# Performance work log

Hardware: AMD Instinct MI355X
Metric: run time of the kernel (lower is better)

Reference implementation:

```python
import jax, jax.numpy as jnp
import numpy as np
from jax import lax

B, T, F_IN = 128, 2048, 8
CF = 128   # cnn_filters
H = 96     # lstm_hidden
NC = 6

def _ln(x, g, b, eps=1e-5):
    m = jnp.mean(x, -1, keepdims=True)
    v = jnp.mean((x - m) ** 2, -1, keepdims=True)
    return (x - m) * lax.rsqrt(v + eps) * g + b

def _bn(x, g, b, m, v, eps=1e-5):
    # eval-mode BatchNorm; x is [B,C,T] (channel axis 1) or [B,C]
    if x.ndim == 3:
        return (x - m[None, :, None]) * lax.rsqrt(v + eps)[None, :, None] * g[None, :, None] + b[None, :, None]
    return (x - m) * lax.rsqrt(v + eps) * g + b

def _lstm_scan(xp, whh, bhh, g_hh, b_hh, g_ho, b_ho):
    # xp: [T, B, 4H] = ln_ih(x @ W_ih.T + b_ih), precomputed (LN is per-timestep)
    bsz = xp.shape[1]
    hh = whh.shape[1]
    def step(carry, xt):
        hx, cx = carry
        gates = xt + _ln(hx @ whh.T + bhh, g_hh, b_hh)
        i, f, g, o = jnp.split(gates, 4, axis=-1)  # torch chunk order: in, forget, cell, out
        cy = jax.nn.sigmoid(f) * cx + jax.nn.sigmoid(i) * jnp.tanh(g)
        hy = jax.nn.sigmoid(o) * jnp.tanh(_ln(cy, g_ho, b_ho))
        return (hy, cy), hy
    init = (jnp.zeros((bsz, hh), xp.dtype), jnp.zeros((bsz, hh), xp.dtype))
    _, hs = lax.scan(step, init, xp)
    return hs  # [T, B, H]

def setup_inputs():
    key = jax.random.key(0)
    ks = iter(jax.random.split(key, 64))
    def rn(shape, scale=1.0):
        return jax.random.normal(next(ks), shape, jnp.float32) * scale
    def ru(shape, lo, hi):
        return jax.random.uniform(next(ks), shape, jnp.float32, lo, hi)
    D = 2 * CF  # lstm input size = 256
    d = {}
    d['x'] = rn((B, T, F_IN))
    d['conv1_w'] = rn((CF, F_IN, 7), 1.0 / np.sqrt(F_IN * 7)); d['conv1_b'] = jnp.zeros((CF,))
    d['bn1_g'] = jnp.ones((CF,)); d['bn1_b'] = jnp.zeros((CF,))
    d['bn1_m'] = rn((CF,), 0.1); d['bn1_v'] = ru((CF,), 0.5, 1.5)
    d['conv2_w'] = rn((2 * CF, CF, 5), 1.0 / np.sqrt(CF * 5)); d['conv2_b'] = jnp.zeros((2 * CF,))
    d['bn2_g'] = jnp.ones((2 * CF,)); d['bn2_b'] = jnp.zeros((2 * CF,))
    d['bn2_m'] = rn((2 * CF,), 0.1); d['bn2_v'] = ru((2 * CF,), 0.5, 1.5)
    s = 1.0 / np.sqrt(H)
    for p in ['f', 'b']:
        d[p + 'wih'] = rn((4 * H, D), s); d[p + 'bih'] = rn((4 * H,), s)
        d[p + 'whh'] = rn((4 * H, H), s); d[p + 'bhh'] = rn((4 * H,), s)
        d[p + 'lnih_g'] = jnp.ones((4 * H,)); d[p + 'lnih_b'] = jnp.zeros((4 * H,))
        d[p + 'lnhh_g'] = jnp.ones((4 * H,)); d[p + 'lnhh_b'] = jnp.zeros((4 * H,))
        d[p + 'lnho_g'] = jnp.ones((H,)); d[p + 'lnho_b'] = jnp.zeros((H,))
    d['attn_w'] = rn((1, 2 * H), 1.0 / np.sqrt(2 * H))
    d['fc1_w'] = rn((256, 2 * H), 1.0 / np.sqrt(2 * H)); d['fc1_b'] = jnp.zeros((256,))
    d['bn3_g'] = jnp.ones((256,)); d['bn3_b'] = jnp.zeros((256,))
    d['bn3_m'] = rn((256,), 0.1); d['bn3_v'] = ru((256,), 0.5, 1.5)
    d['fc2_w'] = rn((NC, 256), 1.0 / np.sqrt(256)); d['fc2_b'] = jnp.zeros((NC,))
    return d

def _forward(x, conv1_w, conv1_b, bn1_g, bn1_b, bn1_m, bn1_v,
             conv2_w, conv2_b, bn2_g, bn2_b, bn2_m, bn2_v,
             fwih, fbih, fwhh, fbhh, flnih_g, flnih_b, flnhh_g, flnhh_b, flnho_g, flnho_b,
             bwih, bbih, bwhh, bbhh, blnih_g, blnih_b, blnhh_g, blnhh_b, blnho_g, blnho_b,
             attn_w, fc1_w, fc1_b, bn3_g, bn3_b, bn3_m, bn3_v, fc2_w, fc2_b):
    dn = ('NCH', 'OIH', 'NCH')
    h = jnp.transpose(x, (0, 2, 1))  # [B, F_IN, T]
    h = lax.conv_general_dilated(h, conv1_w, (1,), [(3, 3)], dimension_numbers=dn) + conv1_b[None, :, None]
    h = jax.nn.relu(_bn(h, bn1_g, bn1_b, bn1_m, bn1_v))
    h = lax.reduce_window(h, -jnp.inf, lax.max, (1, 1, 2), (1, 1, 2), 'VALID')
    h = lax.conv_general_dilated(h, conv2_w, (1,), [(2, 2)], dimension_numbers=dn) + conv2_b[None, :, None]
    h = jax.nn.relu(_bn(h, bn2_g, bn2_b, bn2_m, bn2_v))
    h = lax.reduce_window(h, -jnp.inf, lax.max, (1, 1, 2), (1, 1, 2), 'VALID')
    # Dropout(0.3) -> identity at eval
    seq = jnp.transpose(h, (2, 0, 1))  # [T/4, B, 2*CF]
    xp_f = _ln(seq @ fwih.T + fbih, flnih_g, flnih_b)
    hf = _lstm_scan(xp_f, fwhh, fbhh, flnhh_g, flnhh_b, flnho_g, flnho_b)
    xp_b = _ln(seq @ bwih.T + bbih, blnih_g, blnih_b)[::-1]
    hb = _lstm_scan(xp_b, bwhh, bbhh, blnhh_g, blnhh_b, blnho_g, blnho_b)[::-1]
    lstm_out = jnp.transpose(jnp.concatenate([hf, hb], -1), (1, 0, 2))  # [B, T/4, 2H]
    attn = jax.nn.softmax(lstm_out @ attn_w.T, axis=1)  # [B, T/4, 1]
    ctx = jnp.sum(attn * lstm_out, axis=1)  # [B, 2H]
    h2 = jax.nn.relu(_bn(ctx @ fc1_w.T + fc1_b, bn3_g, bn3_b, bn3_m, bn3_v))
    return h2 @ fc2_w.T + fc2_b  # [B, NC]

def reference(x, conv1_w, conv1_b, bn1_g, bn1_b, bn1_m, bn1_v,
              conv2_w, conv2_b, bn2_g, bn2_b, bn2_m, bn2_v,
              fwih, fbih, fwhh, fbhh, flnih_g, flnih_b, flnhh_g, flnhh_b, flnho_g, flnho_b,
              bwih, bbih, bwhh, bbhh, blnih_g, blnih_b, blnhh_g, blnhh_b, blnho_g, blnho_b,
              attn_w, fc1_w, fc1_b, bn3_g, bn3_b, bn3_m, bn3_v, fc2_w, fc2_b):
    return _forward(x, conv1_w, conv1_b, bn1_g, bn1_b, bn1_m, bn1_v,
                    conv2_w, conv2_b, bn2_g, bn2_b, bn2_m, bn2_v,
                    fwih, fbih, fwhh, fbhh, flnih_g, flnih_b, flnhh_g, flnhh_b, flnho_g, flnho_b,
                    bwih, bbih, bwhh, bbhh, blnih_g, blnih_b, blnhh_g, blnhh_b, blnho_g, blnho_b,
                    attn_w, fc1_w, fc1_b, bn3_g, bn3_b, bn3_m, bn3_v, fc2_w, fc2_b)
```

## Files before the change

### kernel.cpp

```cpp
#include <hip/hip_runtime.h>

typedef unsigned short u16;
typedef unsigned int   u32;
typedef __attribute__((ext_vector_type(8))) short bf16x8;
typedef __attribute__((ext_vector_type(4))) float f32x4;

#define DI __device__ __forceinline__

DI float b2f(u16 u){ union{u32 i; float f;} x; x.i = ((u32)u)<<16; return x.f; }
DI u16 f2bf(float f){ union{float f; u32 i;} x; x.f=f; u32 r = x.i + 0x7FFFu + ((x.i>>16)&1u); return (u16)(r>>16); }
DI float sigf(float x){ return 1.0f/(1.0f + __expf(-x)); }
DI float tanh_(float x){ return 1.0f - 2.0f/(__expf(2.0f*x)+1.0f); }
DI float dot4(float4 a, float4 b){ return a.x*b.x + a.y*b.y + a.z*b.z + a.w*b.w; }

__global__ __launch_bounds__(256) void k_conv1(
    const float* __restrict__ x, const float* __restrict__ w,
    const float* __restrict__ cb, const float* __restrict__ bg, const float* __restrict__ bb,
    const float* __restrict__ bm, const float* __restrict__ bv, u16* __restrict__ out)
{
  __shared__ __align__(16) float xs[262*12];
  __shared__ __align__(16) float wl[128*7*8];
  __shared__ float As[128], Ss[128];
  const int tid = threadIdx.x;
  const int tc  = blockIdx.x;
  const int b   = blockIdx.y;
  const int tau0 = tc*256;
  for(int f = tid; f < 262*8; f += 256){
    int tt = f >> 3;
    int ci = f & 7;
    int xg = tau0 - 3 + tt;
    float val = 0.f;
    if(xg >= 0 && xg < 2048) val = x[(b*2048 + xg)*8 + ci];
    xs[tt*12 + ci] = val;
  }
  for(int d = tid; d < 128*7*8; d += 256){
    int co = d / 56; int r = d - co*56; int k = r >> 3; int ci = r & 7;
    wl[d] = w[(co*8 + ci)*7 + k];
  }
  if(tid < 128){
    float a = bg[tid] * rsqrtf(bv[tid] + 1e-5f);
    As[tid] = a;
    Ss[tid] = (cb[tid] - bm[tid])*a + bb[tid];
  }
  __syncthreads();
  const float4* xs4 = (const float4*)xs;
  const float4* wl4 = (const float4*)wl;
  const int p2  = tid & 63;
  const int grp = tid >> 6;
  float4 ra[10], rb[10];
  #pragma unroll
  for(int e=0; e<10; e++){ ra[e] = xs4[(4*p2+e)*3]; rb[e] = xs4[(4*p2+e)*3 + 1]; }
  u32* out32 = (u32*)out;
  for(int i = 0; i < 32; i++){
    const int co = grp*32 + i;
    float a0=0.f, a1=0.f, a2=0.f, a3=0.f;
    #pragma unroll
    for(int k=0;k<7;k++){
      float4 wa = wl4[(co*7+k)*2], wb2 = wl4[(co*7+k)*2+1];
      a0 += dot4(ra[k],   wa) + dot4(rb[k],   wb2);
      a1 += dot4(ra[k+1], wa) + dot4(rb[k+1], wb2);
      a2 += dot4(ra[k+2], wa) + dot4(rb[k+2], wb2);
      a3 += dot4(ra[k+3], wa) + dot4(rb[k+3], wb2);
    }
    const float Ac = As[co], Sc = Ss[co];
    const float y0 = fmaxf(fmaxf(a0*Ac+Sc, a1*Ac+Sc), 0.f);
    const float y1 = fmaxf(fmaxf(a2*Ac+Sc, a3*Ac+Sc), 0.f);
    out32[((b*128 + co)<<9) + tc*64 + p2] = (u32)f2bf(y0) | ((u32)f2bf(y1) << 16);
  }
}

__global__ __launch_bounds__(256) void k_prep(
    const float* __restrict__ w, u16* __restrict__ wp3)
{
  const int f = blockIdx.x*256 + threadIdx.x;
  const int co = f / 640; const int r = f - co*640;
  const int ci = r / 5;   const int k = r - ci*5;
  const float wv = w[f];
  const u16 h0 = f2bf(wv);
  const float r1 = wv - b2f(h0);
  const u16 h1 = f2bf(r1);
  const float r2 = r1 - b2f(h1);
  const u16 h2 = f2bf(r2);
  const int cib = ci >> 5, cl = ci & 31;
  const int base = (k*4 + cib)*10240 + co*40 + cl;
  wp3[base]                = h0;
  wp3[base +   5*4*10240]  = h1;
  wp3[base + 2*5*4*10240]  = h2;
}

__global__ __launch_bounds__(512) void k_conv2(
    const u16* __restrict__ cin, const u16* __restrict__ wp3,
    const float* __restrict__ cb, const float* __restrict__ bg, const float* __restrict__ bb,
    const float* __restrict__ bm, const float* __restrict__ bv, u16* __restrict__ seq)
{
  __shared__ __align__(16) u16 xsT[260*136];
  __shared__ __align__(16) u16 wb[3][256*40];
  __shared__ float As[256], Ss[256];
  const int tid = threadIdx.x;
  const int tc  = blockIdx.x;
  const int b   = blockIdx.y;
  const int wav = tid >> 6;
  const int rt  = wav & 3;
  const int coh = wav >> 2;
  const int l = tid & 63;
  const int g = l >> 4;
  const int c = l & 15;
  if(tid < 256){
    float a = bg[tid] * rsqrtf(bv[tid] + 1e-5f);
    As[tid] = a; Ss[tid] = (cb[tid] - bm[tid])*a + bb[tid];
  }
  for(int f = tid; f < 33280; f += 512){
    int ci = f / 260, tt = f - ci*260;
    int tg = tc*256 - 2 + tt;
    u16 val = 0;
    if(tg >= 0 && tg < 1024) val = cin[((b*128 + ci)<<10) + tg];
    xsT[tt*136 + ci] = val;
  }
  f32x4 acc[4][8];
  #pragma unroll
  for(int q4=0;q4<4;q4++)
    #pragma unroll
    for(int n=0;n<8;n++) acc[q4][n] = (f32x4){0.f,0.f,0.f,0.f};
  for(int s=0; s<20; s++){
    const int k = s >> 2, cib = s & 3;
    __syncthreads();
    #pragma unroll
    for(int sp=0; sp<3; sp++){
      const uint4* src = (const uint4*)(wp3 + ((sp*5 + k)*4 + cib)*10240);
      uint4* dst = (uint4*)wb[sp];
      for(int f = tid; f < 1280; f += 512) dst[f] = src[f];
    }
    __syncthreads();
    bf16x8 afr[4];
    #pragma unroll
    for(int q4=0;q4<4;q4++)
      afr[q4] = *(const bf16x8*)&xsT[((q4*4 + rt)*16 + c + k)*136 + cib*32 + g*8];
    #pragma unroll
    for(int n=0; n<8; n++){
      bf16x8 b0 = *(const bf16x8*)&wb[0][(coh*128 + n*16 + c)*40 + g*8];
      bf16x8 b1 = *(const bf16x8*)&wb[1][(coh*128 + n*16 + c)*40 + g*8];
      bf16x8 b2 = *(const bf16x8*)&wb[2][(coh*128 + n*16 + c)*40 + g*8];
      #pragma unroll
      for(int q4=0;q4<4;q4++){
        acc[q4][n] = __builtin_amdgcn_mfma_f32_16x16x32_bf16(afr[q4], b0, acc[q4][n], 0, 0, 0);
        acc[q4][n] = __builtin_amdgcn_mfma_f32_16x16x32_bf16(afr[q4], b1, acc[q4][n], 0, 0, 0);
        acc[q4][n] = __builtin_amdgcn_mfma_f32_16x16x32_bf16(afr[q4], b2, acc[q4][n], 0, 0, 0);
      }
    }
  }
  #pragma unroll
  for(int q4=0;q4<4;q4++){
    const int T = q4*4 + rt;
    const int tp0 = tc*128 + T*8 + g*2;
    #pragma unroll
    for(int n=0; n<8; n++){
      int co = coh*128 + n*16 + c;
      float Ac = As[co], Sc = Ss[co];
      float p0 = fmaxf(fmaxf(acc[q4][n][0]*Ac+Sc, acc[q4][n][1]*Ac+Sc), 0.f);
      float p1 = fmaxf(fmaxf(acc[q4][n][2]*Ac+Sc, acc[q4][n][3]*Ac+Sc), 0.f);
      seq[((tp0+0)*128 + b)*256 + co] = f2bf(p0);
      seq[((tp0+1)*128 + b)*256 + co] = f2bf(p1);
    }
  }
}

__global__ __launch_bounds__(512) void k_xp(
    const u16* __restrict__ seq,
    const float* __restrict__ fw, const float* __restrict__ fbi, const float* __restrict__ fg, const float* __restrict__ fb,
    const float* __restrict__ bw, const float* __restrict__ bbi, const float* __restrict__ bg_, const float* __restrict__ bb_,
    u16* __restrict__ xpf, u16* __restrict__ xpb)
{
  __shared__ __align__(16) char lds[104960];
  u16*   wbh  = (u16*)lds;
  u16*   wbl  = (u16*)(lds + 30720);
  u16*   ost  = (u16*)lds;
  float* lnbi = (float*)(lds + 100352);
  float* lng  = lnbi + 384;
  float* lnb2 = lnbi + 768;
  const float *W, *BI, *LG, *LB; u16* out;
  if(blockIdx.y == 0){ W=fw; BI=fbi; LG=fg;  LB=fb;  out=xpf; }
  else               { W=bw; BI=bbi; LG=bg_; LB=bb_; out=xpb; }
  const int tid = threadIdx.x;
  const int row0 = blockIdx.x * 128;
  const int w = tid >> 6;
  const int l = tid & 63;
  const int g = l >> 4;
  const int c = l & 15;
  if(tid < 384){ lnbi[tid] = BI[tid]; lng[tid] = LG[tid]; lnb2[tid] = LB[tid]; }
  const int arow = row0 + w*16 + c;
  bf16x8 afr[8];
  #pragma unroll
  for(int ks=0; ks<8; ks++)
    afr[ks] = *(const bf16x8*)&seq[arow*256 + ks*32 + g*8];
  f32x4 acc[24];
  #pragma unroll
  for(int n=0; n<24; n++) acc[n] = (f32x4){0.f,0.f,0.f,0.f};
  #pragma unroll
  for(int ks=0; ks<8; ks++){
    __syncthreads();
    for(int f = tid; f < 12288; f += 512){
      int jj = f >> 5, kk = f & 31;
      float wv = W[jj*256 + ks*32 + kk];
      u16 hi = f2bf(wv);
      wbh[jj*40 + kk] = hi;
      wbl[jj*40 + kk] = f2bf(wv - b2f(hi));
    }
    __syncthreads();
    #pragma unroll
    for(int n=0; n<24; n++){
      bf16x8 bhi = *(const bf16x8*)&wbh[(n*16 + c)*40 + g*8];
      bf16x8 blo = *(const bf16x8*)&wbl[(n*16 + c)*40 + g*8];
      acc[n] = __builtin_amdgcn_mfma_f32_16x16x32_bf16(afr[ks], bhi, acc[n], 0, 0, 0);
      acc[n] = __builtin_amdgcn_mfma_f32_16x16x32_bf16(afr[ks], blo, acc[n], 0, 0, 0);
    }
  }
  __syncthreads();
  float bic[24];
  #pragma unroll
  for(int n=0; n<24; n++) bic[n] = lnbi[n*16 + c];
  float mean[4], rs[4];
  #pragma unroll
  for(int q=0; q<4; q++){
    float s = 0.f, ss = 0.f;
    #pragma unroll
    for(int n=0; n<24; n++){
      float u = acc[n][q] + bic[n];
      s += u; ss += u*u;
    }
    #pragma unroll
    for(int msk=1; msk<16; msk<<=1){ s += __shfl_xor(s,msk); ss += __shfl_xor(ss,msk); }
    mean[q] = s * (1.f/384.f);
    float var = fmaxf(ss * (1.f/384.f) - mean[q]*mean[q], 0.f);
    rs[q] = rsqrtf(var + 1e-5f);
  }
  #pragma unroll
  for(int n=0; n<24; n++){
    float lgv = lng[n*16 + c], lbv = lnb2[n*16 + c];
    #pragma unroll
    for(int q=0; q<4; q++){
      float u = acc[n][q] + bic[n];
      float y = (u - mean[q])*rs[q]*lgv + lbv;
      ost[(w*16 + g*4 + q)*392 + n*16 + c] = f2bf(y);
    }
  }
  __syncthreads();
  for(int f = tid; f < 6144; f += 512){
    int row = f / 48, ch = f - row*48;
    uint4 v = *(const uint4*)&ost[row*392 + ch*8];
    *(uint4*)&out[(row0 + row)*384 + ch*8] = v;
  }
}

__global__ __launch_bounds__(384) void k_lstm(
    const u16* __restrict__ xpf, const u16* __restrict__ xpb,
    const float* __restrict__ fwhh, const float* __restrict__ fbhh, const float* __restrict__ fgh, const float* __restrict__ fbh2,
    const float* __restrict__ fgho, const float* __restrict__ fbho,
    const float* __restrict__ bwhh, const float* __restrict__ bbhh, const float* __restrict__ bgh, const float* __restrict__ bbh2,
    const float* __restrict__ bgho, const float* __restrict__ bbho,
    u16* __restrict__ hcat)
{
  __shared__ float4 hx4[24];
  __shared__ float gbuf[384];
  __shared__ float red[16];
  const int b   = blockIdx.x;
  const int dir = blockIdx.y;
  const u16* xp;
  const float *whh, *bh, *gh, *bh2, *gho, *bho;
  if(dir == 0){ xp=xpf; whh=fwhh; bh=fbhh; gh=fgh; bh2=fbh2; gho=fgho; bho=fbho; }
  else        { xp=xpb; whh=bwhh; bh=bbhh; gh=bgh; bh2=bbh2; gho=bgho; bho=bbho; }
  const int j = threadIdx.x;
  const int wid = j >> 6;
  float wr[96];
  {
    const float4* wp4 = (const float4*)(whh + j*96);
    #pragma unroll
    for(int kk=0; kk<24; kk++){
      float4 v = wp4[kk];
      wr[4*kk]=v.x; wr[4*kk+1]=v.y; wr[4*kk+2]=v.z; wr[4*kk+3]=v.w;
    }
  }
  const float bh_j = bh[j], gh_j = gh[j], bh2_j = bh2[j];
  float gho_j = 0.f, bho_j = 0.f, cx = 0.f;
  if(j < 96){ gho_j = gho[j]; bho_j = bho[j]; }
  float* hx = (float*)hx4;
  if(j < 96) hx[j] = 0.f;
  __syncthreads();
  for(int t=0; t<512; t++){
    const int ts = dir ? (511 - t) : t;
    const float xt = b2f(xp[(ts*128 + b)*384 + j]);
    float a0=0.f,a1=0.f,a2=0.f,a3=0.f;
    #pragma unroll
    for(int kk=0; kk<24; kk++){
      float4 h4 = hx4[kk];
      a0 += h4.x * wr[4*kk];
      a1 += h4.y * wr[4*kk+1];
      a2 += h4.z * wr[4*kk+2];
      a3 += h4.w * wr[4*kk+3];
    }
    const float u = (a0+a1)+(a2+a3) + bh_j;
    float s = u, ss = u*u;
    #pragma unroll
    for(int msk=32; msk; msk>>=1){ s += __shfl_xor(s,msk); ss += __shfl_xor(ss,msk); }
    if((j & 63) == 0){ red[wid*2] = s; red[wid*2+1] = ss; }
    __syncthreads();
    float S=0.f, SS=0.f;
    #pragma unroll
    for(int wv=0; wv<6; wv++){ S += red[wv*2]; SS += red[wv*2+1]; }
    const float mean = S*(1.f/384.f);
    const float var  = fmaxf(SS*(1.f/384.f) - mean*mean, 0.f);
    const float rs   = rsqrtf(var + 1e-5f);
    const float gate = xt + (u - mean)*rs*gh_j + bh2_j;
    gbuf[j] = gate;
    __syncthreads();
    float cy = 0.f, go_ = 0.f;
    if(j < 128){
      if(j < 96){
        float gi = gbuf[j], gf = gbuf[j+96], gg = gbuf[j+192];
        go_ = gbuf[j+288];
        cy = sigf(gf)*cx + sigf(gi)*tanh_(gg);
        cx = cy;
      }
      float s2 = cy, ss2 = cy*cy;
      #pragma unroll
      for(int msk=32; msk; msk>>=1){ s2 += __shfl_xor(s2,msk); ss2 += __shfl_xor(ss2,msk); }
      if((j & 63) == 0){ red[12 + wid*2] = s2; red[13 + wid*2] = ss2; }
    }
    __syncthreads();
    if(j < 96){
      const float S2 = red[12]+red[14], SS2 = red[13]+red[15];
      const float m2  = S2*(1.f/96.f);
      const float v2  = fmaxf(SS2*(1.f/96.f) - m2*m2, 0.f);
      const float rs2 = rsqrtf(v2 + 1e-5f);
      const float lnho = (cy - m2)*rs2*gho_j + bho_j;
      const float hy = sigf(go_)*tanh_(lnho);
      hx[j] = hy;
      hcat[(ts*128 + b)*192 + dir*96 + j] = f2bf(hy);
    }
    __syncthreads();
  }
}

__global__ __launch_bounds__(256) void k_head(
    const u16* __restrict__ hcat, const float* __restrict__ aw,
    const float* __restrict__ f1w, const float* __restrict__ f1b,
    const float* __restrict__ g3, const float* __restrict__ b3, const float* __restrict__ m3, const float* __restrict__ v3,
    const float* __restrict__ fc2w, const float* __restrict__ fc2bias,
    float* __restrict__ out)
{
  __shared__ float p[512];
  __shared__ float red[8];
  __shared__ __align__(16) float ctx[192];
  __shared__ float h2[256];
  __shared__ float awl[192];
  const int b = blockIdx.x;
  const int tid = threadIdx.x;
  if(tid < 192) awl[tid] = aw[tid];
  __syncthreads();
  float sc0 = 0.f, sc1 = 0.f;
  #pragma unroll
  for(int i=0;i<2;i++){
    int t = i*256 + tid;
    const uint4* hp = (const uint4*)(hcat + (t*128 + b)*192);
    float acc = 0.f;
    #pragma unroll 6
    for(int qq=0;qq<24;qq++){
      uint4 pv = hp[qq];
      acc += b2f((u16)(pv.x&0xffffu))*awl[qq*8+0] + b2f((u16)(pv.x>>16))*awl[qq*8+1]
           + b2f((u16)(pv.y&0xffffu))*awl[qq*8+2] + b2f((u16)(pv.y>>16))*awl[qq*8+3]
           + b2f((u16)(pv.z&0xffffu))*awl[qq*8+4] + b2f((u16)(pv.z>>16))*awl[qq*8+5]
           + b2f((u16)(pv.w&0xffffu))*awl[qq*8+6] + b2f((u16)(pv.w>>16))*awl[qq*8+7];
    }
    if(i==0) sc0 = acc; else sc1 = acc;
  }
  float mx = fmaxf(sc0, sc1);
  for(int msk=32; msk; msk>>=1) mx = fmaxf(mx, __shfl_xor(mx,msk));
  if((tid&63)==0) red[tid>>6] = mx;
  __syncthreads();
  mx = fmaxf(fmaxf(red[0],red[1]), fmaxf(red[2],red[3]));
  float e0 = __expf(sc0-mx), e1 = __expf(sc1-mx);
  float sm = e0 + e1;
  for(int msk=32; msk; msk>>=1) sm += __shfl_xor(sm,msk);
  if((tid&63)==0) red[4 + (tid>>6)] = sm;
  __syncthreads();
  const float inv = 1.f/(red[4]+red[5]+red[6]+red[7]);
  p[tid] = e0*inv; p[tid+256] = e1*inv;
  __syncthreads();
  if(tid < 192){
    float acc = 0.f;
    for(int t=0;t<512;t++){
      acc += p[t] * b2f(hcat[(t*128 + b)*192 + tid]);
    }
    ctx[tid] = acc;
  }
  __syncthreads();
  {
    const float4* cv = (const float4*)ctx;
    const float4* wp = (const float4*)(f1w + tid*192);
    float acc = 0.f;
    #pragma unroll 8
    for(int qq=0;qq<48;qq++){
      acc += dot4(wp[qq], cv[qq]);
    }
    acc += f1b[tid];
    float a = g3[tid] * rsqrtf(v3[tid] + 1e-5f);
    float y = (acc - m3[tid])*a + b3[tid];
    h2[tid] = fmaxf(y, 0.f);
  }
  __syncthreads();
  if(tid < 6){
    float acc = fc2bias[tid];
    for(int k=0;k<256;k++) acc += h2[k]*fc2w[tid*256 + k];
    out[b*6 + tid] = acc;
  }
}

extern "C" void kernel_launch(void* const* d_in, const int* in_sizes, int n_in,
                              void* d_out, int out_size, void* d_ws, size_t ws_size,
                              hipStream_t stream)
{
  (void)in_sizes; (void)n_in; (void)out_size; (void)ws_size;
  const float* X      = (const float*)d_in[0];
  const float* c1w    = (const float*)d_in[1];
  const float* c1b    = (const float*)d_in[2];
  const float* bn1g   = (const float*)d_in[3];
  const float* bn1b   = (const float*)d_in[4];
  const float* bn1m   = (const float*)d_in[5];
  const float* bn1v   = (const float*)d_in[6];
  const float* c2w    = (const float*)d_in[7];
  const float* c2b    = (const float*)d_in[8];
  const float* bn2g   = (const float*)d_in[9];
  const float* bn2b   = (const float*)d_in[10];
  const float* bn2m   = (const float*)d_in[11];
  const float* bn2v   = (const float*)d_in[12];
  const float* fwih   = (const float*)d_in[13];
  const float* fbih   = (const float*)d_in[14];
  const float* fwhh   = (const float*)d_in[15];
  const float* fbhh   = (const float*)d_in[16];
  const float* flnihg = (const float*)d_in[17];
  const float* flnihb = (const float*)d_in[18];
  const float* flnhhg = (const float*)d_in[19];
  const float* flnhhb = (const float*)d_in[20];
  const float* flnhog = (const float*)d_in[21];
  const float* flnhob = (const float*)d_in[22];
  const float* bwih   = (const float*)d_in[23];
  const float* bbih   = (const float*)d_in[24];
  const float* bwhh   = (const float*)d_in[25];
  const float* bbhh   = (const float*)d_in[26];
  const float* blnihg = (const float*)d_in[27];
  const float* blnihb = (const float*)d_in[28];
  const float* blnhhg = (const float*)d_in[29];
  const float* blnhhb = (const float*)d_in[30];
  const float* blnhog = (const float*)d_in[31];
  const float* blnhob = (const float*)d_in[32];
  const float* attnw  = (const float*)d_in[33];
  const float* fc1w   = (const float*)d_in[34];
  const float* fc1b   = (const float*)d_in[35];
  const float* bn3g   = (const float*)d_in[36];
  const float* bn3b   = (const float*)d_in[37];
  const float* bn3m   = (const float*)d_in[38];
  const float* bn3v   = (const float*)d_in[39];
  const float* fc2w   = (const float*)d_in[40];
  const float* fc2b_  = (const float*)d_in[41];

  char* ws = (char*)d_ws;
  const size_t MB = 1048576;
  u16* seq   = (u16*)(ws);
  u16* xpf   = (u16*)(ws + 32*MB);
  u16* xpb   = (u16*)(ws + 80*MB);
  u16* wprep = (u16*)(ws + 80*MB);
  u16* c1o   = (u16*)(ws + 96*MB);
  u16* hcat  = (u16*)(ws);

  k_prep <<<dim3(640),    256, 0, stream>>>(c2w, wprep);
  k_conv1<<<dim3(8,128),  256, 0, stream>>>(X,   c1w, c1b, bn1g, bn1b, bn1m, bn1v, c1o);
  k_conv2<<<dim3(4,128),  512, 0, stream>>>(c1o, wprep, c2b, bn2g, bn2b, bn2m, bn2v, seq);
  k_xp  <<<dim3(512,2),   512, 0, stream>>>(seq, fwih, fbih, flnihg, flnihb,
                                                 bwih, bbih, blnihg, blnihb, xpf, xpb);
  k_lstm<<<dim3(128,2),   384, 0, stream>>>(xpf, xpb,
      fwhh, fbhh, flnhhg, flnhhb, flnhog, flnhob,
      bwhh, bbhh, blnhhg, blnhhb, blnhog, blnhob, hcat);
  k_head<<<dim3(128),     256, 0, stream>>>(hcat, attnw, fc1w, fc1b,
      bn3g, bn3b, bn3m, bn3v, fc2w, fc2b_, (float*)d_out);
}
```

Measured before the change: 1.547 ms.

## Double-buffer weight staging in k_xp and prefetch/batch LSTM I/O

In k_xp, the bf16 hi/lo weight slices are now double-buffered in LDS. The next k-slice is staged while MFMAs consume the current one, which removes one barrier per iteration at the cost of more shared memory (about 127 KB). In k_lstm, the next timestep's input projection is prefetched into a register to hide global load latency on the serial recurrence. Hidden-state outputs are buffered in LDS for 8 steps and then written as 16-byte vector stores instead of scattered 2-byte stores. The larger LDS footprint in k_xp may reduce occupancy.

```diff
diff --git a/kernel.cpp b/kernel.cpp
--- a/kernel.cpp
+++ b/kernel.cpp
@@ -170,11 +170,9 @@
     const float* __restrict__ bw, const float* __restrict__ bbi, const float* __restrict__ bg_, const float* __restrict__ bb_,
     u16* __restrict__ xpf, u16* __restrict__ xpb)
 {
-  __shared__ __align__(16) char lds[104960];
-  u16*   wbh  = (u16*)lds;
-  u16*   wbl  = (u16*)(lds + 30720);
+  __shared__ __align__(16) char lds[127488];
   u16*   ost  = (u16*)lds;
-  float* lnbi = (float*)(lds + 100352);
+  float* lnbi = (float*)(lds + 122880);
   float* lng  = lnbi + 384;
   float* lnb2 = lnbi + 768;
   const float *W, *BI, *LG, *LB; u16* out;
@@ -195,26 +193,34 @@
   f32x4 acc[24];
   #pragma unroll
   for(int n=0; n<24; n++) acc[n] = (f32x4){0.f,0.f,0.f,0.f};
+  #define STAGE_W(KS, BB) { \
+    u16* wh = (u16*)(lds + ((BB)*2+0)*30720); \
+    u16* wl2 = (u16*)(lds + ((BB)*2+1)*30720); \
+    for(int f = tid; f < 12288; f += 512){ \
+      int jj = f >> 5, kk = f & 31; \
+      float wv = W[jj*256 + (KS)*32 + kk]; \
+      u16 hi = f2bf(wv); \
+      wh[jj*40 + kk] = hi; \
+      wl2[jj*40 + kk] = f2bf(wv - b2f(hi)); \
+    } }
+  STAGE_W(0, 0)
+  __syncthreads();
   #pragma unroll
   for(int ks=0; ks<8; ks++){
-    __syncthreads();
-    for(int f = tid; f < 12288; f += 512){
-      int jj = f >> 5, kk = f & 31;
-      float wv = W[jj*256 + ks*32 + kk];
-      u16 hi = f2bf(wv);
-      wbh[jj*40 + kk] = hi;
-      wbl[jj*40 + kk] = f2bf(wv - b2f(hi));
-    }
-    __syncthreads();
+    const int cur = ks & 1;
+    if(ks < 7) STAGE_W(ks+1, cur^1)
+    const u16* wh = (const u16*)(lds + (cur*2+0)*30720);
+    const u16* wl2 = (const u16*)(lds + (cur*2+1)*30720);
     #pragma unroll
     for(int n=0; n<24; n++){
-      bf16x8 bhi = *(const bf16x8*)&wbh[(n*16 + c)*40 + g*8];
-      bf16x8 blo = *(const bf16x8*)&wbl[(n*16 + c)*40 + g*8];
+      bf16x8 bhi = *(const bf16x8*)&wh[(n*16 + c)*40 + g*8];
+      bf16x8 blo = *(const bf16x8*)&wl2[(n*16 + c)*40 + g*8];
       acc[n] = __builtin_amdgcn_mfma_f32_16x16x32_bf16(afr[ks], bhi, acc[n], 0, 0, 0);
       acc[n] = __builtin_amdgcn_mfma_f32_16x16x32_bf16(afr[ks], blo, acc[n], 0, 0, 0);
     }
-  }
-  __syncthreads();
+    __syncthreads();
+  }
+  #undef STAGE_W
   float bic[24];
   #pragma unroll
   for(int n=0; n<24; n++) bic[n] = lnbi[n*16 + c];
@@ -262,6 +268,7 @@
   __shared__ float4 hx4[24];
   __shared__ float gbuf[384];
   __shared__ float red[16];
+  __shared__ __align__(16) u16 hstage[8][96];
   const int b   = blockIdx.x;
   const int dir = blockIdx.y;
   const u16* xp;
@@ -284,10 +291,14 @@
   if(j < 96){ gho_j = gho[j]; bho_j = bho[j]; }
   float* hx = (float*)hx4;
   if(j < 96) hx[j] = 0.f;
+  const u16* xrow = xp + b*384 + j;
+  u16 xt_u = xrow[(dir ? 511 : 0)*49152];
   __syncthreads();
   for(int t=0; t<512; t++){
     const int ts = dir ? (511 - t) : t;
-    const float xt = b2f(xp[(ts*128 + b)*384 + j]);
+    u16 xn = 0;
+    if(t < 511) xn = xrow[(dir ? (510 - t) : (t + 1))*49152];
+    const float xt = b2f(xt_u);
     float a0=0.f,a1=0.f,a2=0.f,a3=0.f;
     #pragma unroll
     for(int kk=0; kk<24; kk++){
@@ -334,9 +345,19 @@
       const float lnho = (cy - m2)*rs2*gho_j + bho_j;
       const float hy = sigf(go_)*tanh_(lnho);
       hx[j] = hy;
-      hcat[(ts*128 + b)*192 + dir*96 + j] = f2bf(hy);
-    }
-    __syncthreads();
+      hstage[t & 7][j] = f2bf(hy);
+    }
+    xt_u = xn;
+    __syncthreads();
+    if((t & 7) == 7){
+      if(j < 96){
+        const int row = j / 12, ch = j - row*12;
+        const int tt = (t - 7) + row;
+        const int tsr = dir ? (511 - tt) : tt;
+        uint4 v = *(const uint4*)&hstage[row][ch*8];
+        *(uint4*)&hcat[(tsr*128 + b)*192 + dir*96 + ch*8] = v;
+      }
+    }
   }
 }
 
```

Result: no change. 1.547 ms (+0.0%).

## Fuse conv2 with LSTM input projection and prefetch/stage LSTM I/O

Applied to the files above, without the earlier changes.

Merges the conv2 kernel and the LSTM input-projection kernel into one kernel. The conv2 output tile stays in LDS and feeds both direction projections directly, so the bf16 sequence buffer no longer makes a round trip through global memory. The separate conv2 weight prep kernel is removed and its three-way bf16 split is now done inline, once per block per stage. The LSTM kernel prefetches the next timestep's input and buffers 8 hidden states in LDS before writing them out with vector stores. In exchange, the weight conversion is repeated across every block and the fused kernel uses much more LDS (about 139KB), which lowers occupancy and serialises the two projection directions inside each block.

```diff
diff --git a/kernel.cpp b/kernel.cpp
--- a/kernel.cpp
+++ b/kernel.cpp
@@ -69,33 +69,28 @@
   }
 }
 
-__global__ __launch_bounds__(256) void k_prep(
-    const float* __restrict__ w, u16* __restrict__ wp3)
+__global__ __launch_bounds__(512) void k_c2xp(
+    const u16* __restrict__ cin, const float* __restrict__ w2,
+    const float* __restrict__ cb, const float* __restrict__ bg, const float* __restrict__ bb,
+    const float* __restrict__ bm, const float* __restrict__ bv,
+    const float* __restrict__ fw, const float* __restrict__ fbi, const float* __restrict__ fg, const float* __restrict__ fb,
+    const float* __restrict__ bw, const float* __restrict__ bbi, const float* __restrict__ bg_, const float* __restrict__ bb_,
+    u16* __restrict__ xpf, u16* __restrict__ xpb)
 {
-  const int f = blockIdx.x*256 + threadIdx.x;
-  const int co = f / 640; const int r = f - co*640;
-  const int ci = r / 5;   const int k = r - ci*5;
-  const float wv = w[f];
-  const u16 h0 = f2bf(wv);
-  const float r1 = wv - b2f(h0);
-  const u16 h1 = f2bf(r1);
-  const float r2 = r1 - b2f(h1);
-  const u16 h2 = f2bf(r2);
-  const int cib = ci >> 5, cl = ci & 31;
-  const int base = (k*4 + cib)*10240 + co*40 + cl;
-  wp3[base]                = h0;
-  wp3[base +   5*4*10240]  = h1;
-  wp3[base + 2*5*4*10240]  = h2;
-}
-
-__global__ __launch_bounds__(512) void k_conv2(
-    const u16* __restrict__ cin, const u16* __restrict__ wp3,
-    const float* __restrict__ cb, const float* __restrict__ bg, const float* __restrict__ bb,
-    const float* __restrict__ bm, const float* __restrict__ bv, u16* __restrict__ seq)
-{
-  __shared__ __align__(16) u16 xsT[260*136];
-  __shared__ __align__(16) u16 wb[3][256*40];
-  __shared__ float As[256], Ss[256];
+  __shared__ __align__(16) char lds[138816];
+  u16*   xsT  = (u16*)lds;
+  u16*   wb0  = (u16*)(lds + 70720);
+  u16*   wb1  = (u16*)(lds + 91200);
+  u16*   wb2s = (u16*)(lds + 111680);
+  float* As   = (float*)(lds + 132160);
+  float* Ss   = (float*)(lds + 133184);
+  u16*   seqL = (u16*)lds;
+  u16*   wbh  = (u16*)(lds + 70720);
+  u16*   wbl  = (u16*)(lds + 101440);
+  u16*   ost  = (u16*)(lds + 70720);
+  float* lnbi = (float*)(lds + 134208);
+  float* lng  = lnbi + 384;
+  float* lnb2 = lnbi + 768;
   const int tid = threadIdx.x;
   const int tc  = blockIdx.x;
   const int b   = blockIdx.y;
@@ -124,130 +119,124 @@
   for(int s=0; s<20; s++){
     const int k = s >> 2, cib = s & 3;
     __syncthreads();
-    #pragma unroll
-    for(int sp=0; sp<3; sp++){
-      const uint4* src = (const uint4*)(wp3 + ((sp*5 + k)*4 + cib)*10240);
-      uint4* dst = (uint4*)wb[sp];
-      for(int f = tid; f < 1280; f += 512) dst[f] = src[f];
-    }
-    __syncthreads();
-    bf16x8 afr[4];
+    for(int f = tid; f < 8192; f += 512){
+      int co = f >> 5, cl = f & 31;
+      float wvv = w2[co*640 + (cib*32 + cl)*5 + k];
+      u16 h0 = f2bf(wvv);
+      float r1 = wvv - b2f(h0);
+      u16 h1 = f2bf(r1);
+      float r2 = r1 - b2f(h1);
+      wb0[co*40 + cl] = h0;
+      wb1[co*40 + cl] = h1;
+      wb2s[co*40 + cl] = f2bf(r2);
+    }
+    __syncthreads();
+    bf16x8 afr2[4];
     #pragma unroll
     for(int q4=0;q4<4;q4++)
-      afr[q4] = *(const bf16x8*)&xsT[((q4*4 + rt)*16 + c + k)*136 + cib*32 + g*8];
+      afr2[q4] = *(const bf16x8*)&xsT[((q4*4 + rt)*16 + c + k)*136 + cib*32 + g*8];
     #pragma unroll
     for(int n=0; n<8; n++){
-      bf16x8 b0 = *(const bf16x8*)&wb[0][(coh*128 + n*16 + c)*40 + g*8];
-      bf16x8 b1 = *(const bf16x8*)&wb[1][(coh*128 + n*16 + c)*40 + g*8];
-      bf16x8 b2 = *(const bf16x8*)&wb[2][(coh*128 + n*16 + c)*40 + g*8];
+      bf16x8 b0 = *(const bf16x8*)&wb0[(coh*128 + n*16 + c)*40 + g*8];
+      bf16x8 b1 = *(const bf16x8*)&wb1[(coh*128 + n*16 + c)*40 + g*8];
+      bf16x8 b2 = *(const bf16x8*)&wb2s[(coh*128 + n*16 + c)*40 + g*8];
       #pragma unroll
       for(int q4=0;q4<4;q4++){
-        acc[q4][n] = __builtin_amdgcn_mfma_f32_16x16x32_bf16(afr[q4], b0, acc[q4][n], 0, 0, 0);
-        acc[q4][n] = __builtin_amdgcn_mfma_f32_16x16x32_bf16(afr[q4], b1, acc[q4][n], 0, 0, 0);
-        acc[q4][n] = __builtin_amdgcn_mfma_f32_16x16x32_bf16(afr[q4], b2, acc[q4][n], 0, 0, 0);
-      }
-    }
-  }
+        acc[q4][n] = __builtin_amdgcn_mfma_f32_16x16x32_bf16(afr2[q4], b0, acc[q4][n], 0, 0, 0);
+        acc[q4][n] = __builtin_amdgcn_mfma_f32_16x16x32_bf16(afr2[q4], b1, acc[q4][n], 0, 0, 0);
+        acc[q4][n] = __builtin_amdgcn_mfma_f32_16x16x32_bf16(afr2[q4], b2, acc[q4][n], 0, 0, 0);
+      }
+    }
+  }
+  __syncthreads();
   #pragma unroll
   for(int q4=0;q4<4;q4++){
     const int T = q4*4 + rt;
-    const int tp0 = tc*128 + T*8 + g*2;
+    const int tpl = T*8 + g*2;
     #pragma unroll
     for(int n=0; n<8; n++){
       int co = coh*128 + n*16 + c;
       float Ac = As[co], Sc = Ss[co];
       float p0 = fmaxf(fmaxf(acc[q4][n][0]*Ac+Sc, acc[q4][n][1]*Ac+Sc), 0.f);
       float p1 = fmaxf(fmaxf(acc[q4][n][2]*Ac+Sc, acc[q4][n][3]*Ac+Sc), 0.f);
-      seq[((tp0+0)*128 + b)*256 + co] = f2bf(p0);
-      seq[((tp0+1)*128 + b)*256 + co] = f2bf(p1);
-    }
-  }
-}
-
-__global__ __launch_bounds__(512) void k_xp(
-    const u16* __restrict__ seq,
-    const float* __restrict__ fw, const float* __restrict__ fbi, const float* __restrict__ fg, const float* __restrict__ fb,
-    const float* __restrict__ bw, const float* __restrict__ bbi, const float* __restrict__ bg_, const float* __restrict__ bb_,
-    u16* __restrict__ xpf, u16* __restrict__ xpb)
-{
-  __shared__ __align__(16) char lds[104960];
-  u16*   wbh  = (u16*)lds;
-  u16*   wbl  = (u16*)(lds + 30720);
-  u16*   ost  = (u16*)lds;
-  float* lnbi = (float*)(lds + 100352);
-  float* lng  = lnbi + 384;
-  float* lnb2 = lnbi + 768;
-  const float *W, *BI, *LG, *LB; u16* out;
-  if(blockIdx.y == 0){ W=fw; BI=fbi; LG=fg;  LB=fb;  out=xpf; }
-  else               { W=bw; BI=bbi; LG=bg_; LB=bb_; out=xpb; }
-  const int tid = threadIdx.x;
-  const int row0 = blockIdx.x * 128;
-  const int w = tid >> 6;
-  const int l = tid & 63;
-  const int g = l >> 4;
-  const int c = l & 15;
-  if(tid < 384){ lnbi[tid] = BI[tid]; lng[tid] = LG[tid]; lnb2[tid] = LB[tid]; }
-  const int arow = row0 + w*16 + c;
+      seqL[(tpl+0)*264 + co] = f2bf(p0);
+      seqL[(tpl+1)*264 + co] = f2bf(p1);
+    }
+  }
+  __syncthreads();
   bf16x8 afr[8];
   #pragma unroll
   for(int ks=0; ks<8; ks++)
-    afr[ks] = *(const bf16x8*)&seq[arow*256 + ks*32 + g*8];
-  f32x4 acc[24];
-  #pragma unroll
-  for(int n=0; n<24; n++) acc[n] = (f32x4){0.f,0.f,0.f,0.f};
-  #pragma unroll
-  for(int ks=0; ks<8; ks++){
-    __syncthreads();
-    for(int f = tid; f < 12288; f += 512){
-      int jj = f >> 5, kk = f & 31;
-      float wv = W[jj*256 + ks*32 + kk];
-      u16 hi = f2bf(wv);
-      wbh[jj*40 + kk] = hi;
-      wbl[jj*40 + kk] = f2bf(wv - b2f(hi));
-    }
-    __syncthreads();
-    #pragma unroll
-    for(int n=0; n<24; n++){
-      bf16x8 bhi = *(const bf16x8*)&wbh[(n*16 + c)*40 + g*8];
-      bf16x8 blo = *(const bf16x8*)&wbl[(n*16 + c)*40 + g*8];
-      acc[n] = __builtin_amdgcn_mfma_f32_16x16x32_bf16(afr[ks], bhi, acc[n], 0, 0, 0);
-      acc[n] = __builtin_amdgcn_mfma_f32_16x16x32_bf16(afr[ks], blo, acc[n], 0, 0, 0);
-    }
-  }
-  __syncthreads();
-  float bic[24];
-  #pragma unroll
-  for(int n=0; n<24; n++) bic[n] = lnbi[n*16 + c];
-  float mean[4], rs[4];
-  #pragma unroll
-  for(int q=0; q<4; q++){
-    float s = 0.f, ss = 0.f;
-    #pragma unroll
-    for(int n=0; n<24; n++){
-      float u = acc[n][q] + bic[n];
-      s += u; ss += u*u;
-    }
-    #pragma unroll
-    for(int msk=1; msk<16; msk<<=1){ s += __shfl_xor(s,msk); ss += __shfl_xor(ss,msk); }
-    mean[q] = s * (1.f/384.f);
-    float var = fmaxf(ss * (1.f/384.f) - mean[q]*mean[q], 0.f);
-    rs[q] = rsqrtf(var + 1e-5f);
-  }
-  #pragma unroll
-  for(int n=0; n<24; n++){
-    float lgv = lng[n*16 + c], lbv = lnb2[n*16 + c];
+    afr[ks] = *(const bf16x8*)&seqL[(wav*16 + c)*264 + ks*32 + g*8];
+  for(int d=0; d<2; d++){
+    const float *W  = d ? bw  : fw;
+    const float *BI = d ? bbi : fbi;
+    const float *LG = d ? bg_ : fg;
+    const float *LB = d ? bb_ : fb;
+    u16* outp = d ? xpb : xpf;
+    __syncthreads();
+    if(tid < 384){ lnbi[tid] = BI[tid]; lng[tid] = LG[tid]; lnb2[tid] = LB[tid]; }
+    f32x4 axc[24];
+    #pragma unroll
+    for(int n=0; n<24; n++) axc[n] = (f32x4){0.f,0.f,0.f,0.f};
+    for(int ks=0; ks<8; ks++){
+      if(ks) __syncthreads();
+      for(int f = tid; f < 12288; f += 512){
+        int jj = f >> 5, kk = f & 31;
+        float wvv = W[jj*256 + ks*32 + kk];
+        u16 hi = f2bf(wvv);
+        wbh[jj*40 + kk] = hi;
+        wbl[jj*40 + kk] = f2bf(wvv - b2f(hi));
+      }
+      __syncthreads();
+      #pragma unroll
+      for(int n=0; n<24; n++){
+        bf16x8 bhi = *(const bf16x8*)&wbh[(n*16 + c)*40 + g*8];
+        bf16x8 blo = *(const bf16x8*)&wbl[(n*16 + c)*40 + g*8];
+        axc[n] = __builtin_amdgcn_mfma_f32_16x16x32_bf16(afr[ks], bhi, axc[n], 0, 0, 0);
+        axc[n] = __builtin_amdgcn_mfma_f32_16x16x32_bf16(afr[ks], blo, axc[n], 0, 0, 0);
+      }
+    }
+    float bic[24];
+    #pragma unroll
+    for(int n=0; n<24; n++) bic[n] = lnbi[n*16 + c];
+    float mean[4], rs[4];
     #pragma unroll
     for(int q=0; q<4; q++){
-      float u = acc[n][q] + bic[n];
-      float y = (u - mean[q])*rs[q]*lgv + lbv;
-      ost[(w*16 + g*4 + q)*392 + n*16 + c] = f2bf(y);
-    }
-  }
-  __syncthreads();
-  for(int f = tid; f < 6144; f += 512){
-    int row = f / 48, ch = f - row*48;
-    uint4 v = *(const uint4*)&ost[row*392 + ch*8];
-    *(uint4*)&out[(row0 + row)*384 + ch*8] = v;
+      float s = 0.f, ss = 0.f;
+      #pragma unroll
+      for(int n=0; n<24; n++){
+        float u = axc[n][q] + bic[n];
+        s += u; ss += u*u;
+      }
+      #pragma unroll
+      for(int msk=1; msk<16; msk<<=1){ s += __shfl_xor(s,msk); ss += __shfl_xor(ss,msk); }
+      mean[q] = s * (1.f/384.f);
+      float var = fmaxf(ss * (1.f/384.f) - mean[q]*mean[q], 0.f);
+      rs[q] = rsqrtf(var + 1e-5f);
+    }
+    for(int h=0; h<2; h++){
+      __syncthreads();
+      if((wav >> 2) == h){
+        #pragma unroll
+        for(int n=0; n<24; n++){
+          float lgv = lng[n*16 + c], lbv = lnb2[n*16 + c];
+          #pragma unroll
+          for(int q=0; q<4; q++){
+            float u = axc[n][q] + bic[n];
+            float y = (u - mean[q])*rs[q]*lgv + lbv;
+            ost[((wav&3)*16 + g*4 + q)*392 + n*16 + c] = f2bf(y);
+          }
+        }
+      }
+      __syncthreads();
+      for(int f2 = tid; f2 < 3072; f2 += 512){
+        int r64 = f2 / 48, ch = f2 - r64*48;
+        int grow = (tc*128 + h*64 + r64)*128 + b;
+        uint4 v = *(const uint4*)&ost[r64*392 + ch*8];
+        *(uint4*)&outp[grow*384 + ch*8] = v;
+      }
+    }
   }
 }
 
@@ -262,6 +251,7 @@
   __shared__ float4 hx4[24];
   __shared__ float gbuf[384];
   __shared__ float red[16];
+  __shared__ __align__(16) u16 hstage[8][96];
   const int b   = blockIdx.x;
   const int dir = blockIdx.y;
   const u16* xp;
@@ -284,10 +274,14 @@
   if(j < 96){ gho_j = gho[j]; bho_j = bho[j]; }
   float* hx = (float*)hx4;
   if(j < 96) hx[j] = 0.f;
+  const u16* xrow = xp + b*384 + j;
+  u16 xt_u = xrow[(dir ? 511 : 0)*49152];
   __syncthreads();
   for(int t=0; t<512; t++){
     const int ts = dir ? (511 - t) : t;
-    const float xt = b2f(xp[(ts*128 + b)*384 + j]);
+    u16 xn = 0;
+    if(t < 511) xn = xrow[(dir ? (510 - t) : (t + 1))*49152];
+    const float xt = b2f(xt_u);
     float a0=0.f,a1=0.f,a2=0.f,a3=0.f;
     #pragma unroll
     for(int kk=0; kk<24; kk++){
@@ -334,9 +328,19 @@
       const float lnho = (cy - m2)*rs2*gho_j + bho_j;
       const float hy = sigf(go_)*tanh_(lnho);
       hx[j] = hy;
-      hcat[(ts*128 + b)*192 + dir*96 + j] = f2bf(hy);
-    }
-    __syncthreads();
+      hstage[t & 7][j] = f2bf(hy);
+    }
+    xt_u = xn;
+    __syncthreads();
+    if((t & 7) == 7){
+      if(j < 96){
+        const int row = j / 12, ch = j - row*12;
+        const int tt = (t - 7) + row;
+        const int tsr = dir ? (511 - tt) : tt;
+        uint4 v = *(const uint4*)&hstage[row][ch*8];
+        *(uint4*)&hcat[(tsr*128 + b)*192 + dir*96 + ch*8] = v;
+      }
+    }
   }
 }
 
@@ -464,21 +468,17 @@
 
   char* ws = (char*)d_ws;
   const size_t MB = 1048576;
-  u16* seq   = (u16*)(ws);
-  u16* xpf   = (u16*)(ws + 32*MB);
-  u16* xpb   = (u16*)(ws + 80*MB);
-  u16* wprep = (u16*)(ws + 80*MB);
-  u16* c1o   = (u16*)(ws + 96*MB);
-  u16* hcat  = (u16*)(ws);
-
-  k_prep <<<dim3(640),    256, 0, stream>>>(c2w, wprep);
-  k_conv1<<<dim3(8,128),  256, 0, stream>>>(X,   c1w, c1b, bn1g, bn1b, bn1m, bn1v, c1o);
-  k_conv2<<<dim3(4,128),  512, 0, stream>>>(c1o, wprep, c2b, bn2g, bn2b, bn2m, bn2v, seq);
-  k_xp  <<<dim3(512,2),   512, 0, stream>>>(seq, fwih, fbih, flnihg, flnihb,
-                                                 bwih, bbih, blnihg, blnihb, xpf, xpb);
-  k_lstm<<<dim3(128,2),   384, 0, stream>>>(xpf, xpb,
+  u16* c1o  = (u16*)(ws);
+  u16* xpf  = (u16*)(ws + 32*MB);
+  u16* xpb  = (u16*)(ws + 80*MB);
+  u16* hcat = (u16*)(ws);
+
+  k_conv1<<<dim3(8,128),  256, 0, stream>>>(X, c1w, c1b, bn1g, bn1b, bn1m, bn1v, c1o);
+  k_c2xp <<<dim3(4,128),  512, 0, stream>>>(c1o, c2w, c2b, bn2g, bn2b, bn2m, bn2v,
+      fwih, fbih, flnihg, flnihb, bwih, bbih, blnihg, blnihb, xpf, xpb);
+  k_lstm <<<dim3(128,2),  384, 0, stream>>>(xpf, xpb,
       fwhh, fbhh, flnhhg, flnhhb, flnhog, flnhob,
       bwhh, bbhh, blnhhg, blnhhb, blnhog, blnhob, hcat);
-  k_head<<<dim3(128),     256, 0, stream>>>(hcat, attnw, fc1w, fc1b,
+  k_head <<<dim3(128),    256, 0, stream>>>(hcat, attnw, fc1w, fc1b,
       bn3g, bn3b, bn3m, bn3v, fc2w, fc2b_, (float*)d_out);
 }
```

Measured after the change: 1.630 ms. 1.05x slower.
